# Kernel tuning notes

Hardware: AMD Instinct MI355X
Metric: run time of the kernel (lower is better)

The kernel has to match this reference:

```python
import jax, jax.numpy as jnp
import numpy as np

N, C, T, V = 16, 192, 120, 100
HEADS = 4
HEAD_CH = C // HEADS  # 48


def setup_inputs() -> dict:
    key = jax.random.key(0)
    ks = jax.random.split(key, 10)
    s = 0.05
    return {
        "x_q": jax.random.normal(ks[0], (N, C, T, V), jnp.float32),
        "x_kv": jax.random.normal(ks[1], (N, C, T, V), jnp.float32),
        "wq": jax.random.normal(ks[2], (C, C), jnp.float32) * s,
        "bq": jax.random.normal(ks[3], (C,), jnp.float32) * s,
        "wk": jax.random.normal(ks[4], (C, C), jnp.float32) * s,
        "bk": jax.random.normal(ks[5], (C,), jnp.float32) * s,
        "wp": jax.random.normal(ks[6], (C, C * HEADS), jnp.float32) * s,
        "bp": jax.random.normal(ks[7], (C,), jnp.float32) * s,
        "alphas": jnp.ones((1, HEADS, 1, 1), jnp.float32),
        "global_attn": jax.random.normal(ks[8], (1, 1, V, V), jnp.float32) * s,
    }


def reference(x_q, x_kv, wq, bq, wk, bk, wp, bp, alphas, global_attn):
    n, c, t, v = x_q.shape
    # 1x1 conv == pointwise linear over channel dim
    q = jnp.einsum('oc,nctv->notv', wq, x_q) + bq[None, :, None, None]
    k = jnp.einsum('oc,nctv->notv', wk, x_kv) + bk[None, :, None, None]
    q = q.reshape(n, HEADS, HEAD_CH, t, v)
    k = k.reshape(n, HEADS, HEAD_CH, t, v)
    # scores over (head_ch, T) contraction -> (N, heads, V, V)
    attn = jnp.tanh(jnp.einsum('nsctu,nsctv->nsuv', q, k) / (HEAD_CH * t))
    attn = attn * alphas + global_attn
    # aggregate full-channel x_kv per head: (N, heads, C, T, V)
    values = jnp.einsum('nctu,nsuv->nsctv', x_kv, attn)
    values = values.reshape(n, HEADS * c, t, v)
    out = jnp.einsum('oc,nctv->notv', wp, values) + bp[None, :, None, None]
    return out
```

## Files before the change

### kernel.cpp

```cpp
#include <hip/hip_runtime.h>

#define NN 16
#define CC 192
#define TT 120
#define VV 100
#define NH 4

typedef __attribute__((ext_vector_type(4))) float  float4v;
typedef __attribute__((ext_vector_type(8))) short  short8;
typedef __attribute__((ext_vector_type(2))) int    int2v;

#define MFMA16(A,B,Cacc) __builtin_amdgcn_mfma_f32_16x16x32_bf16(A,B,Cacc,0,0,0)

union S8U { unsigned u[4]; short8 s; };

__device__ __forceinline__ unsigned pk2(float a, float b) {
  union { float f; unsigned u; } x, y; x.f = a; y.f = b;
  return __builtin_amdgcn_perm(y.u, x.u, 0x07060302u);
}
__device__ __forceinline__ short b16t(float f) {
  union { float f; unsigned u; } x; x.f = f;
  return (short)(x.u >> 16);
}
__device__ __forceinline__ short f2b(float f) {
  union { float f; unsigned u; } x; x.f = f;
  unsigned r = x.u + 0x7fffu + ((x.u >> 16) & 1u);
  return (short)(r >> 16);
}

__global__ __launch_bounds__(256) void k_conv(const float* __restrict__ wq,
                                              const float* __restrict__ wk,
                                              const float* __restrict__ wp,
                                              short* __restrict__ wqF,
                                              short* __restrict__ wkF,
                                              short* __restrict__ wpF) {
  int i = blockIdx.x * 256 + threadIdx.x;
  if (i < CC*CC) {
    int o = i / CC, a = i % CC;
    int ct = o >> 4, l = o & 15, kc = a >> 5, q = (a & 31) >> 3, j = a & 7;
    int dst = ((ct*6 + kc)*64 + q*16 + l)*8 + j;
    wqF[dst] = f2b(wq[i]);
    wkF[dst] = f2b(wk[i]);
  }
  if (i < CC*CC*NH) {
    int o = i / (CC*NH), c2 = i % (CC*NH);
    int s = c2 / CC, cc = c2 % CC;
    int T = o >> 4, l = o & 15, kc = cc >> 5, q = (cc & 31) >> 3, j = cc & 7;
    int dst = (((s*12 + T)*6 + kc)*64 + q*16 + l)*8 + j;
    wpF[dst] = f2b(wp[i]);
  }
}

__global__ __launch_bounds__(448, 4) void k_qk(const float* __restrict__ xq,
                                               const float* __restrict__ xkv,
                                               const short* __restrict__ wqF,
                                               const short* __restrict__ wkF,
                                               const float* __restrict__ bq,
                                               const float* __restrict__ bk,
                                               short* __restrict__ Qf,
                                               short* __restrict__ Kf) {
  const int n = blockIdx.x / TT, t = blockIdx.x % TT;
  const int tid = threadIdx.x, w = tid >> 6, lane = tid & 63;
  const int q = lane >> 4, l15 = lane & 15;
  const int u = 16*w + l15, uc = (u < VV) ? u : (VV-1);
  const size_t ns0 = (size_t)n*NH;

  #pragma unroll 1
  for (int ph = 0; ph < 2; ++ph) {
    const float* xb   = (ph ? xkv : xq) + (size_t)n*CC*TT*VV + t*VV;
    const short* wF   = ph ? wkF : wqF;
    const float* bias = ph ? bk : bq;
    short*       Of   = ph ? Kf : Qf;

    short8 xf[6];
    #pragma unroll
    for (int kc = 0; kc < 6; ++kc) {
      float f[8];
      #pragma unroll
      for (int j = 0; j < 8; ++j)
        f[j] = xb[(size_t)(32*kc + 8*q + j)*(TT*VV) + uc];
      S8U sv; sv.u[0]=pk2(f[0],f[1]); sv.u[1]=pk2(f[2],f[3]); sv.u[2]=pk2(f[4],f[5]); sv.u[3]=pk2(f[6],f[7]);
      xf[kc] = sv.s;
    }
    #pragma unroll
    for (int ct = 0; ct < 12; ++ct) {
      float4v d = (float4v){0.f,0.f,0.f,0.f};
      #pragma unroll
      for (int kc = 0; kc < 6; ++kc) {
        short8 wf = *(const short8*)&wF[((ct*6 + kc)*64 + lane)*8];
        d = MFMA16(wf, xf[kc], d);
      }
      const float4v bv = *(const float4v*)&bias[16*ct + 4*q];
      const int sH = ct/3;
      const int kb = 48*t + 16*(ct - 3*sH);
      const int kq = kb + 4*q;
      const int kk = kq >> 5, q2 = (kq >> 3) & 3, j2 = kq & 7;
      size_t base = ((((ns0 + sH)*7 + w)*180 + kk)*64 + (q2*16 + l15))*8 + j2;
      int2v pr;
      pr.x = (int)pk2(d[0] + bv[0], d[1] + bv[1]);
      pr.y = (int)pk2(d[2] + bv[2], d[3] + bv[3]);
      *(int2v*)&Of[base] = pr;
    }
  }
}

__global__ __launch_bounds__(448, 4) void k_scores3(const short* __restrict__ Qf,
                                                    const short* __restrict__ Kf,
                                                    float* __restrict__ part2) {
  const int b = blockIdx.x;
  const int vh = b & 1, kc = (b >> 1) % 6, ns = b / 12;
  const int tid = threadIdx.x, w = tid >> 6, lane = tid & 63;
  const int q = lane >> 4, l15 = lane & 15;
  const short* Qb = Qf + (((size_t)ns*7 + w)*180 + kc*30)*512 + lane*8;
  const short* Kb = Kf + ((size_t)ns*7*180 + kc*30)*512 + lane*8;
  const int vt0 = vh ? 4 : 0, nvt = vh ? 3 : 4;

  float4v acc[4];
  #pragma unroll
  for (int j = 0; j < 4; ++j) acc[j] = (float4v){0.f,0.f,0.f,0.f};

  #pragma unroll 2
  for (int kk = 0; kk < 30; ++kk) {
    short8 aQ = *(const short8*)&Qb[(size_t)kk*512];
    #pragma unroll
    for (int j = 0; j < 4; ++j) {
      if (j < nvt) {
        short8 bK = *(const short8*)&Kb[((size_t)(vt0 + j)*180 + kk)*512];
        acc[j] = MFMA16(aQ, bK, acc[j]);
      }
    }
  }
  #pragma unroll
  for (int j = 0; j < 4; ++j) {
    if (j < nvt) {
      size_t p2 = (((size_t)ns*6 + kc)*112 + 16*(vt0 + j) + l15)*112 + 16*w + 4*q;
      __builtin_nontemporal_store(acc[j], (float4v*)&part2[p2]);
    }
  }
}

__global__ __launch_bounds__(256) void k_reduce2(const float* __restrict__ part2,
                                                 const float* __restrict__ alphas,
                                                 const float* __restrict__ ga,
                                                 short* __restrict__ attnT) {
  int bid = blockIdx.x;
  int ns = bid / 56, vc = bid % 56;
  int v = vc*2 + (threadIdx.x >> 7), u = threadIdx.x & 127;
  int s = ns & 3;
  float val = 0.f;
  if (v < VV && u < VV) {
    float sum = 0.f;
    #pragma unroll
    for (int kc = 0; kc < 6; ++kc)
      sum += __builtin_nontemporal_load(&part2[(((size_t)ns*6 + kc)*112 + v)*112 + u]);
    val = tanhf(sum * (1.f/5760.f)) * alphas[s] + ga[u*VV + v];
  }
  attnT[((size_t)ns*112 + v)*128 + u] = f2b(val);
}

__global__ __launch_bounds__(448, 2) void k_scoresB(const float* __restrict__ xq,
                                                    const float* __restrict__ xkv,
                                                    const short* __restrict__ wqF,
                                                    const short* __restrict__ wkF,
                                                    const float* __restrict__ bq,
                                                    const float* __restrict__ bk,
                                                    float* __restrict__ part) {
  __shared__ short QT[112*200];
  __shared__ short KT[112*56];
  const int n = blockIdx.x / 15, tc = blockIdx.x % 15;
  const int tid = threadIdx.x, w = tid >> 6, lane = tid & 63;
  const int q = lane >> 4, l15 = lane & 15;
  const int u = 16*w + l15, uc = (u < VV) ? u : (VV-1);
  float4v acc[NH][7];
  #pragma unroll
  for (int s = 0; s < NH; ++s)
    #pragma unroll
    for (int vt = 0; vt < 7; ++vt) acc[s][vt] = (float4v){0.f,0.f,0.f,0.f};
  const short8 z8 = {0,0,0,0,0,0,0,0};
  #pragma unroll 1
  for (int it = 0; it < 8; ++it) {
    const int t = tc*8 + it;
    short8 xf[6];
    #pragma unroll
    for (int kc = 0; kc < 6; ++kc) {
      float f[8];
      #pragma unroll
      for (int j = 0; j < 8; ++j)
        f[j] = xq[(n*CC + 32*kc + 8*q + j)*(TT*VV) + t*VV + uc];
      S8U sv; sv.u[0]=pk2(f[0],f[1]); sv.u[1]=pk2(f[2],f[3]); sv.u[2]=pk2(f[4],f[5]); sv.u[3]=pk2(f[6],f[7]);
      xf[kc] = sv.s;
    }
    #pragma unroll
    for (int ct = 0; ct < 12; ++ct) {
      float4v d = (float4v){0.f,0.f,0.f,0.f};
      #pragma unroll
      for (int kc = 0; kc < 6; ++kc) {
        short8 wf = *(const short8*)&wqF[((ct*6 + kc)*64 + q*16 + l15)*8];
        d = MFMA16(xf[kc], wf, d);
      }
      float bb = bq[16*ct + l15];
      #pragma unroll
      for (int r = 0; r < 4; ++r)
        QT[(16*w + 4*q + r)*200 + 16*ct + l15] = b16t(d[r] + bb);
    }
    short8 xg[6];
    #pragma unroll
    for (int kc = 0; kc < 6; ++kc) {
      float f[8];
      #pragma unroll
      for (int j = 0; j < 8; ++j)
        f[j] = xkv[(n*CC + 32*kc + 8*q + j)*(TT*VV) + t*VV + uc];
      S8U sv; sv.u[0]=pk2(f[0],f[1]); sv.u[1]=pk2(f[2],f[3]); sv.u[2]=pk2(f[4],f[5]); sv.u[3]=pk2(f[6],f[7]);
      xg[kc] = sv.s;
    }
    #pragma unroll 1
    for (int s = 0; s < NH; ++s) {
      #pragma unroll
      for (int ctk = 0; ctk < 3; ++ctk) {
        float4v d = (float4v){0.f,0.f,0.f,0.f};
        #pragma unroll
        for (int kc = 0; kc < 6; ++kc) {
          short8 wf = *(const short8*)&wkF[(((3*s + ctk)*6 + kc)*64 + q*16 + l15)*8];
          d = MFMA16(xg[kc], wf, d);
        }
        float bb = bk[48*s + 16*ctk + l15];
        #pragma unroll
        for (int r = 0; r < 4; ++r)
          KT[(16*w + 4*q + r)*56 + 16*ctk + l15] = b16t(d[r] + bb);
      }
      __syncthreads();
      #pragma unroll
      for (int kcp = 0; kcp < 2; ++kcp) {
        short8 aQ = z8;
        if (kcp == 0 || q < 2)
          aQ = *(const short8*)&QT[(16*w + l15)*200 + 48*s + 32*kcp + 8*q];
        #pragma unroll
        for (int vt = 0; vt < 7; ++vt) {
          short8 bK = z8;
          if (kcp == 0 || q < 2)
            bK = *(const short8*)&KT[(16*vt + l15)*56 + 32*kcp + 8*q];
          acc[s][vt] = MFMA16(aQ, bK, acc[s][vt]);
        }
      }
      __syncthreads();
    }
  }
  #pragma unroll
  for (int s = 0; s < NH; ++s)
    #pragma unroll
    for (int vt = 0; vt < 7; ++vt) {
      int v = 16*vt + l15;
      if (v < VV)
        __builtin_nontemporal_store(acc[s][vt],
          (float4v*)&part[(((n*15 + tc)*NH + s)*VV + v)*112 + 16*w + 4*q]);
    }
}

__global__ __launch_bounds__(256) void k_reduce(const float* __restrict__ part,
                                                const float* __restrict__ alphas,
                                                const float* __restrict__ ga,
                                                short* __restrict__ attnT) {
  int bid = blockIdx.x;
  int n = bid / 224, rem = bid % 224, s = rem / 56, vc = rem % 56;
  int v = vc*2 + (threadIdx.x >> 7), uu = threadIdx.x & 127;
  float val = 0.f;
  if (v < VV && uu < VV) {
    float sum = 0.f;
    for (int tcc = 0; tcc < 15; ++tcc)
      sum += __builtin_nontemporal_load(&part[(((n*15 + tcc)*NH + s)*VV + v)*112 + uu]);
    val = tanhf(sum * (1.f/5760.f)) * alphas[s] + ga[uu*VV + v];
  }
  attnT[((n*NH + s)*112 + v)*128 + uu] = f2b(val);
}

__global__ __launch_bounds__(256, 2) void k_outE(const float* __restrict__ xkv,
                                                 const short* __restrict__ wpF,
                                                 const short* __restrict__ attnT,
                                                 const float* __restrict__ bp,
                                                 float* __restrict__ out) {
  __shared__ short YT[112*200];
  const int n = blockIdx.x / TT, t = blockIdx.x % TT;
  const int tid = threadIdx.x, w = tid >> 6, lane = tid & 63;
  const int q = lane >> 4, l15 = lane & 15;

  float4v accO[3][7];
  #pragma unroll
  for (int i = 0; i < 3; ++i)
    #pragma unroll
    for (int vt = 0; vt < 7; ++vt) accO[i][vt] = (float4v){0.f,0.f,0.f,0.f};

  short8   xh[3][3];
  unsigned xt3[3][2];
  #pragma unroll
  for (int i = 0; i < 3; ++i) {
    const float* xb = xkv + ((size_t)(n*CC + 16*(w + 4*i) + l15)*TT + t)*VV;
    #pragma unroll
    for (int ku = 0; ku < 3; ++ku) {
      const float4v A = *(const float4v*)(xb + 32*ku + 8*q);
      const float4v B = *(const float4v*)(xb + 32*ku + 8*q + 4);
      S8U sv; sv.u[0]=pk2(A[0],A[1]); sv.u[1]=pk2(A[2],A[3]);
      sv.u[2]=pk2(B[0],B[1]); sv.u[3]=pk2(B[2],B[3]);
      xh[i][ku] = sv.s;
    }
    if (q == 0) {
      const float4v A = *(const float4v*)(xb + 96);
      xt3[i][0] = pk2(A[0],A[1]); xt3[i][1] = pk2(A[2],A[3]);
    } else { xt3[i][0] = 0u; xt3[i][1] = 0u; }
  }

  #pragma unroll 1
  for (int s = 0; s < NH; ++s) {
    const short* aT = attnT + (size_t)((n*NH + s)*112)*128;

    __syncthreads();
    #pragma unroll
    for (int vt = 0; vt < 7; ++vt) {
      float4v y0 = (float4v){0.f,0.f,0.f,0.f};
      float4v y1 = y0, y2 = y0;
      #pragma unroll
      for (int ku = 0; ku < 4; ++ku) {
        short8 bv = *(const short8*)&aT[(16*vt + l15)*128 + 32*ku + 8*q];
        short8 a0, a1, a2;
        if (ku < 3) { a0 = xh[0][ku]; a1 = xh[1][ku]; a2 = xh[2][ku]; }
        else {
          S8U s0, s1, s2;
          s0.u[0]=xt3[0][0]; s0.u[1]=xt3[0][1]; s0.u[2]=0u; s0.u[3]=0u;
          s1.u[0]=xt3[1][0]; s1.u[1]=xt3[1][1]; s1.u[2]=0u; s1.u[3]=0u;
          s2.u[0]=xt3[2][0]; s2.u[1]=xt3[2][1]; s2.u[2]=0u; s2.u[3]=0u;
          a0 = s0.s; a1 = s1.s; a2 = s2.s;
        }
        y0 = MFMA16(a0, bv, y0);
        y1 = MFMA16(a1, bv, y1);
        y2 = MFMA16(a2, bv, y2);
      }
      int2v p0; p0.x = (int)pk2(y0[0], y0[1]); p0.y = (int)pk2(y0[2], y0[3]);
      int2v p1; p1.x = (int)pk2(y1[0], y1[1]); p1.y = (int)pk2(y1[2], y1[3]);
      int2v p2; p2.x = (int)pk2(y2[0], y2[1]); p2.y = (int)pk2(y2[2], y2[3]);
      *(int2v*)&YT[(16*vt + l15)*200 + 16*w + 4*q]       = p0;
      *(int2v*)&YT[(16*vt + l15)*200 + 16*(w + 4) + 4*q] = p1;
      *(int2v*)&YT[(16*vt + l15)*200 + 16*(w + 8) + 4*q] = p2;
    }
    __syncthreads();

    #pragma unroll
    for (int kc2 = 0; kc2 < 6; ++kc2) {
      short8 ya[7];
      #pragma unroll
      for (int vt = 0; vt < 7; ++vt)
        ya[vt] = *(const short8*)&YT[(16*vt + l15)*200 + 32*kc2 + 8*q];
      #pragma unroll
      for (int i = 0; i < 3; ++i) {
        short8 wf = *(const short8*)&wpF[(((s*12 + (w + 4*i))*6 + kc2)*64 + q*16 + l15)*8];
        #pragma unroll
        for (int vt = 0; vt < 7; ++vt)
          accO[i][vt] = MFMA16(ya[vt], wf, accO[i][vt]);
      }
    }
  }

  #pragma unroll
  for (int i = 0; i < 3; ++i) {
    int o = 16*(w + 4*i) + l15;
    float b = bp[o];
    #pragma unroll
    for (int vt = 0; vt < 7; ++vt) {
      int v0 = 16*vt + 4*q;
      if (v0 < VV) {
        float4v r = accO[i][vt];
        r[0] += b; r[1] += b; r[2] += b; r[3] += b;
        *(float4v*)&out[((size_t)(n*CC + o)*TT + t)*VV + v0] = r;
      }
    }
  }
}

extern "C" void kernel_launch(void* const* d_in, const int* in_sizes, int n_in,
                              void* d_out, int out_size, void* d_ws, size_t ws_size,
                              hipStream_t stream) {
  const float* xq     = (const float*)d_in[0];
  const float* xkv    = (const float*)d_in[1];
  const float* wq     = (const float*)d_in[2];
  const float* bq     = (const float*)d_in[3];
  const float* wk     = (const float*)d_in[4];
  const float* bk     = (const float*)d_in[5];
  const float* wp     = (const float*)d_in[6];
  const float* bp     = (const float*)d_in[7];
  const float* alphas = (const float*)d_in[8];
  const float* ga     = (const float*)d_in[9];
  float* out = (float*)d_out;
  char*  ws  = (char*)d_ws;

  short* wqF   = (short*)(ws);
  short* wkF   = (short*)(ws + 73728);
  short* wpF   = (short*)(ws + 147456);
  short* attnT = (short*)(ws + 442368);

  hipLaunchKernelGGL(k_conv, dim3(576), dim3(256), 0, stream, wq, wk, wp, wqF, wkF, wpF);

  if (ws_size >= 186695680ULL) {
    short* Qf    = (short*)(ws + 2277376);
    short* Kf    = (short*)(ws + 84852736ULL);
    float* part2 = (float*)(ws + 167428096ULL);
    hipLaunchKernelGGL(k_qk,      dim3(1920), dim3(448), 0, stream, xq, xkv, wqF, wkF, bq, bk, Qf, Kf);
    hipLaunchKernelGGL(k_scores3, dim3(768),  dim3(448), 0, stream, Qf, Kf, part2);
    hipLaunchKernelGGL(k_reduce2, dim3(3584), dim3(256), 0, stream, part2, alphas, ga, attnT);
  } else {
    float* part = (float*)(ws + 2277376);
    hipLaunchKernelGGL(k_scoresB, dim3(240),  dim3(448), 0, stream, xq, xkv, wqF, wkF, bq, bk, part);
    hipLaunchKernelGGL(k_reduce,  dim3(3584), dim3(256), 0, stream, part, alphas, ga, attnT);
  }

  hipLaunchKernelGGL(k_outE, dim3(1920), dim3(256), 0, stream, xkv, wpF, attnT, bp, out);
}
```

Before: 800.7 us.

## Stage Q/K inputs through LDS with coalesced loads; swizzle YT buffer

The Q/K projection kernel now loads each x slice with coalesced float2 reads into a shared-memory transpose buffer instead of strided per-lane channel gathers, then reads MFMA fragments from LDS. The output kernel's YT staging buffer drops its padding and uses an XOR swizzle to avoid LDS bank conflicts. The fallback path (k_scoresB/k_reduce) is removed and the large-workspace path is always used. This adds barriers and LDS usage per block, which may reduce occupancy, and drops the small-workspace fallback.

```diff
diff --git a/kernel.cpp b/kernel.cpp
--- a/kernel.cpp
+++ b/kernel.cpp
@@ -51,18 +51,18 @@
   }
 }
 
-__global__ __launch_bounds__(448, 4) void k_qk(const float* __restrict__ xq,
-                                               const float* __restrict__ xkv,
-                                               const short* __restrict__ wqF,
-                                               const short* __restrict__ wkF,
-                                               const float* __restrict__ bq,
-                                               const float* __restrict__ bk,
-                                               short* __restrict__ Qf,
-                                               short* __restrict__ Kf) {
+__global__ __launch_bounds__(448, 4) void k_qkS(const float* __restrict__ xq,
+                                                const float* __restrict__ xkv,
+                                                const short* __restrict__ wqF,
+                                                const short* __restrict__ wkF,
+                                                const float* __restrict__ bq,
+                                                const float* __restrict__ bk,
+                                                short* __restrict__ Qf,
+                                                short* __restrict__ Kf) {
+  __shared__ short XT[112*200];
   const int n = blockIdx.x / TT, t = blockIdx.x % TT;
   const int tid = threadIdx.x, w = tid >> 6, lane = tid & 63;
   const int q = lane >> 4, l15 = lane & 15;
-  const int u = 16*w + l15, uc = (u < VV) ? u : (VV-1);
   const size_t ns0 = (size_t)n*NH;
 
   #pragma unroll 1
@@ -72,16 +72,23 @@
     const float* bias = ph ? bk : bq;
     short*       Of   = ph ? Kf : Qf;
 
+    if (ph) __syncthreads();
+    #pragma unroll 1
+    for (int idx = tid; idx < 192*56; idx += 448) {
+      int c = idx / 56, p = idx - c*56;
+      int u = 2*p;
+      int us = (u <= 98) ? u : 98;
+      float2 f = *(const float2*)&xb[(size_t)c*(TT*VV) + us];
+      XT[u*200 + c]       = b16t(f.x);
+      XT[(u+1)*200 + c]   = b16t(f.y);
+    }
+    __syncthreads();
+
     short8 xf[6];
     #pragma unroll
-    for (int kc = 0; kc < 6; ++kc) {
-      float f[8];
-      #pragma unroll
-      for (int j = 0; j < 8; ++j)
-        f[j] = xb[(size_t)(32*kc + 8*q + j)*(TT*VV) + uc];
-      S8U sv; sv.u[0]=pk2(f[0],f[1]); sv.u[1]=pk2(f[2],f[3]); sv.u[2]=pk2(f[4],f[5]); sv.u[3]=pk2(f[6],f[7]);
-      xf[kc] = sv.s;
-    }
+    for (int kc = 0; kc < 6; ++kc)
+      xf[kc] = *(const short8*)&XT[(16*w + l15)*200 + 32*kc + 8*q];
+
     #pragma unroll
     for (int ct = 0; ct < 12; ++ct) {
       float4v d = (float4v){0.f,0.f,0.f,0.f};
@@ -158,130 +165,16 @@
   attnT[((size_t)ns*112 + v)*128 + u] = f2b(val);
 }
 
-__global__ __launch_bounds__(448, 2) void k_scoresB(const float* __restrict__ xq,
-                                                    const float* __restrict__ xkv,
-                                                    const short* __restrict__ wqF,
-                                                    const short* __restrict__ wkF,
-                                                    const float* __restrict__ bq,
-                                                    const float* __restrict__ bk,
-                                                    float* __restrict__ part) {
-  __shared__ short QT[112*200];
-  __shared__ short KT[112*56];
-  const int n = blockIdx.x / 15, tc = blockIdx.x % 15;
-  const int tid = threadIdx.x, w = tid >> 6, lane = tid & 63;
-  const int q = lane >> 4, l15 = lane & 15;
-  const int u = 16*w + l15, uc = (u < VV) ? u : (VV-1);
-  float4v acc[NH][7];
-  #pragma unroll
-  for (int s = 0; s < NH; ++s)
-    #pragma unroll
-    for (int vt = 0; vt < 7; ++vt) acc[s][vt] = (float4v){0.f,0.f,0.f,0.f};
-  const short8 z8 = {0,0,0,0,0,0,0,0};
-  #pragma unroll 1
-  for (int it = 0; it < 8; ++it) {
-    const int t = tc*8 + it;
-    short8 xf[6];
-    #pragma unroll
-    for (int kc = 0; kc < 6; ++kc) {
-      float f[8];
-      #pragma unroll
-      for (int j = 0; j < 8; ++j)
-        f[j] = xq[(n*CC + 32*kc + 8*q + j)*(TT*VV) + t*VV + uc];
-      S8U sv; sv.u[0]=pk2(f[0],f[1]); sv.u[1]=pk2(f[2],f[3]); sv.u[2]=pk2(f[4],f[5]); sv.u[3]=pk2(f[6],f[7]);
-      xf[kc] = sv.s;
-    }
-    #pragma unroll
-    for (int ct = 0; ct < 12; ++ct) {
-      float4v d = (float4v){0.f,0.f,0.f,0.f};
-      #pragma unroll
-      for (int kc = 0; kc < 6; ++kc) {
-        short8 wf = *(const short8*)&wqF[((ct*6 + kc)*64 + q*16 + l15)*8];
-        d = MFMA16(xf[kc], wf, d);
-      }
-      float bb = bq[16*ct + l15];
-      #pragma unroll
-      for (int r = 0; r < 4; ++r)
-        QT[(16*w + 4*q + r)*200 + 16*ct + l15] = b16t(d[r] + bb);
-    }
-    short8 xg[6];
-    #pragma unroll
-    for (int kc = 0; kc < 6; ++kc) {
-      float f[8];
-      #pragma unroll
-      for (int j = 0; j < 8; ++j)
-        f[j] = xkv[(n*CC + 32*kc + 8*q + j)*(TT*VV) + t*VV + uc];
-      S8U sv; sv.u[0]=pk2(f[0],f[1]); sv.u[1]=pk2(f[2],f[3]); sv.u[2]=pk2(f[4],f[5]); sv.u[3]=pk2(f[6],f[7]);
-      xg[kc] = sv.s;
-    }
-    #pragma unroll 1
-    for (int s = 0; s < NH; ++s) {
-      #pragma unroll
-      for (int ctk = 0; ctk < 3; ++ctk) {
-        float4v d = (float4v){0.f,0.f,0.f,0.f};
-        #pragma unroll
-        for (int kc = 0; kc < 6; ++kc) {
-          short8 wf = *(const short8*)&wkF[(((3*s + ctk)*6 + kc)*64 + q*16 + l15)*8];
-          d = MFMA16(xg[kc], wf, d);
-        }
-        float bb = bk[48*s + 16*ctk + l15];
-        #pragma unroll
-        for (int r = 0; r < 4; ++r)
-          KT[(16*w + 4*q + r)*56 + 16*ctk + l15] = b16t(d[r] + bb);
-      }
-      __syncthreads();
-      #pragma unroll
-      for (int kcp = 0; kcp < 2; ++kcp) {
-        short8 aQ = z8;
-        if (kcp == 0 || q < 2)
-          aQ = *(const short8*)&QT[(16*w + l15)*200 + 48*s + 32*kcp + 8*q];
-        #pragma unroll
-        for (int vt = 0; vt < 7; ++vt) {
-          short8 bK = z8;
-          if (kcp == 0 || q < 2)
-            bK = *(const short8*)&KT[(16*vt + l15)*56 + 32*kcp + 8*q];
-          acc[s][vt] = MFMA16(aQ, bK, acc[s][vt]);
-        }
-      }
-      __syncthreads();
-    }
-  }
-  #pragma unroll
-  for (int s = 0; s < NH; ++s)
-    #pragma unroll
-    for (int vt = 0; vt < 7; ++vt) {
-      int v = 16*vt + l15;
-      if (v < VV)
-        __builtin_nontemporal_store(acc[s][vt],
-          (float4v*)&part[(((n*15 + tc)*NH + s)*VV + v)*112 + 16*w + 4*q]);
-    }
-}
-
-__global__ __launch_bounds__(256) void k_reduce(const float* __restrict__ part,
-                                                const float* __restrict__ alphas,
-                                                const float* __restrict__ ga,
-                                                short* __restrict__ attnT) {
-  int bid = blockIdx.x;
-  int n = bid / 224, rem = bid % 224, s = rem / 56, vc = rem % 56;
-  int v = vc*2 + (threadIdx.x >> 7), uu = threadIdx.x & 127;
-  float val = 0.f;
-  if (v < VV && uu < VV) {
-    float sum = 0.f;
-    for (int tcc = 0; tcc < 15; ++tcc)
-      sum += __builtin_nontemporal_load(&part[(((n*15 + tcc)*NH + s)*VV + v)*112 + uu]);
-    val = tanhf(sum * (1.f/5760.f)) * alphas[s] + ga[uu*VV + v];
-  }
-  attnT[((n*NH + s)*112 + v)*128 + uu] = f2b(val);
-}
-
 __global__ __launch_bounds__(256, 2) void k_outE(const float* __restrict__ xkv,
                                                  const short* __restrict__ wpF,
                                                  const short* __restrict__ attnT,
                                                  const float* __restrict__ bp,
                                                  float* __restrict__ out) {
-  __shared__ short YT[112*200];
+  __shared__ short YT[112*192];
   const int n = blockIdx.x / TT, t = blockIdx.x % TT;
   const int tid = threadIdx.x, w = tid >> 6, lane = tid & 63;
   const int q = lane >> 4, l15 = lane & 15;
+  const unsigned swz = (unsigned)(l15 & 7) << 4;
 
   float4v accO[3][7];
   #pragma unroll
@@ -336,9 +229,10 @@
       int2v p0; p0.x = (int)pk2(y0[0], y0[1]); p0.y = (int)pk2(y0[2], y0[3]);
       int2v p1; p1.x = (int)pk2(y1[0], y1[1]); p1.y = (int)pk2(y1[2], y1[3]);
       int2v p2; p2.x = (int)pk2(y2[0], y2[1]); p2.y = (int)pk2(y2[2], y2[3]);
-      *(int2v*)&YT[(16*vt + l15)*200 + 16*w + 4*q]       = p0;
-      *(int2v*)&YT[(16*vt + l15)*200 + 16*(w + 4) + 4*q] = p1;
-      *(int2v*)&YT[(16*vt + l15)*200 + 16*(w + 8) + 4*q] = p2;
+      unsigned bw = ((unsigned)(((16*vt + l15)*192 + 16*w + 4*q)*2)) ^ swz;
+      *(int2v*)((char*)YT + bw)       = p0;
+      *(int2v*)((char*)YT + bw + 128) = p1;
+      *(int2v*)((char*)YT + bw + 256) = p2;
     }
     __syncthreads();
 
@@ -346,8 +240,10 @@
     for (int kc2 = 0; kc2 < 6; ++kc2) {
       short8 ya[7];
       #pragma unroll
-      for (int vt = 0; vt < 7; ++vt)
-        ya[vt] = *(const short8*)&YT[(16*vt + l15)*200 + 32*kc2 + 8*q];
+      for (int vt = 0; vt < 7; ++vt) {
+        unsigned br = ((unsigned)(((16*vt + l15)*192 + 32*kc2 + 8*q)*2)) ^ swz;
+        ya[vt] = *(const short8*)((char*)YT + br);
+      }
       #pragma unroll
       for (int i = 0; i < 3; ++i) {
         short8 wf = *(const short8*)&wpF[(((s*12 + (w + 4*i))*6 + kc2)*64 + q*16 + l15)*8];
@@ -394,21 +290,13 @@
   short* wkF   = (short*)(ws + 73728);
   short* wpF   = (short*)(ws + 147456);
   short* attnT = (short*)(ws + 442368);
-
-  hipLaunchKernelGGL(k_conv, dim3(576), dim3(256), 0, stream, wq, wk, wp, wqF, wkF, wpF);
-
-  if (ws_size >= 186695680ULL) {
-    short* Qf    = (short*)(ws + 2277376);
-    short* Kf    = (short*)(ws + 84852736ULL);
-    float* part2 = (float*)(ws + 167428096ULL);
-    hipLaunchKernelGGL(k_qk,      dim3(1920), dim3(448), 0, stream, xq, xkv, wqF, wkF, bq, bk, Qf, Kf);
-    hipLaunchKernelGGL(k_scores3, dim3(768),  dim3(448), 0, stream, Qf, Kf, part2);
-    hipLaunchKernelGGL(k_reduce2, dim3(3584), dim3(256), 0, stream, part2, alphas, ga, attnT);
-  } else {
-    float* part = (float*)(ws + 2277376);
-    hipLaunchKernelGGL(k_scoresB, dim3(240),  dim3(448), 0, stream, xq, xkv, wqF, wkF, bq, bk, part);
-    hipLaunchKernelGGL(k_reduce,  dim3(3584), dim3(256), 0, stream, part, alphas, ga, attnT);
-  }
-
-  hipLaunchKernelGGL(k_outE, dim3(1920), dim3(256), 0, stream, xkv, wpF, attnT, bp, out);
-}
+  short* Qf    = (short*)(ws + 2277376);
+  short* Kf    = (short*)(ws + 84852736ULL);
+  float* part2 = (float*)(ws + 167428096ULL);
+
+  hipLaunchKernelGGL(k_conv,    dim3(576),  dim3(256), 0, stream, wq, wk, wp, wqF, wkF, wpF);
+  hipLaunchKernelGGL(k_qkS,     dim3(1920), dim3(448), 0, stream, xq, xkv, wqF, wkF, bq, bk, Qf, Kf);
+  hipLaunchKernelGGL(k_scores3, dim3(768),  dim3(448), 0, stream, Qf, Kf, part2);
+  hipLaunchKernelGGL(k_reduce2, dim3(3584), dim3(256), 0, stream, part2, alphas, ga, attnT);
+  hipLaunchKernelGGL(k_outE,    dim3(1920), dim3(256), 0, stream, xkv, wpF, attnT, bp, out);
+}
```

Measured after the change: 814.2 us. About the same (+1.7%).
